# Optimization experiments

Hardware: AMD Instinct MI355X
Metric: run time of the kernel (lower is better)

The kernel has to match this reference:

```python
import jax, jax.numpy as jnp
import numpy as np

N, E, G = 100000, 1600000, 256      # nodes, edges, graphs in batch
IN_C, HID, OUT_C = 4, 128, 120
ALPHA = 0.5


def setup_inputs() -> dict:
    key = jax.random.key(0)
    ks = jax.random.split(key, 12)
    def w(k, i, o):
        return jax.random.normal(k, (i, o), jnp.float32) / np.float32(np.sqrt(i))
    return {
        "x": jax.random.normal(ks[0], (N, IN_C), jnp.float32),
        "edge_index": jax.random.randint(ks[1], (2, E), 0, N),
        "batch_seg": jnp.sort(jax.random.randint(ks[2], (N,), 0, G)),
        # DirGNNConv holds two independent GCNConvs (in / reversed direction)
        "W_in": w(ks[3], IN_C, HID),  "b_in": jnp.zeros((HID,), jnp.float32),
        "W_in_r": w(ks[4], IN_C, HID), "b_in_r": jnp.zeros((HID,), jnp.float32),
        "W_mid": w(ks[5], HID, HID),  "b_mid": jnp.zeros((HID,), jnp.float32),
        "W_mid_r": w(ks[6], HID, HID), "b_mid_r": jnp.zeros((HID,), jnp.float32),
        "W_out": w(ks[7], HID, OUT_C), "b_out": jnp.zeros((OUT_C,), jnp.float32),
        "W_out_r": w(ks[8], HID, OUT_C), "b_out_r": jnp.zeros((OUT_C,), jnp.float32),
    }


def _gcn(x, W, b, src, dst, n):
    # GCNConv with add_self_loops=False (DirGNNConv disables self-loops):
    # deg computed on destination side, norm = deg^-1/2[src] * deg^-1/2[dst]
    deg = jax.ops.segment_sum(jnp.ones(src.shape[0], x.dtype), dst, num_segments=n)
    dinv = jnp.where(deg > 0, jax.lax.rsqrt(jnp.maximum(deg, 1e-12)), 0.0)
    h = x @ W                                  # [N, out]
    msg = h[src] * (dinv[src] * dinv[dst])[:, None]  # gather + edge-normalize
    return jax.ops.segment_sum(msg, dst, num_segments=n) + b


def _dir_conv(x, Wi, bi, Wr, br, src, dst):
    # DirGNNConv(root_weight=False): (1-a)*conv(edge_index) + a*conv(flipped)
    n = x.shape[0]
    x_in = _gcn(x, Wi, bi, src, dst, n)
    x_out = _gcn(x, Wr, br, dst, src, n)
    return ALPHA * x_out + (1.0 - ALPHA) * x_in


def reference(x, edge_index, batch_seg, W_in, b_in, W_in_r, b_in_r,
              W_mid, b_mid, W_mid_r, b_mid_r, W_out, b_out, W_out_r, b_out_r):
    src, dst = edge_index[0], edge_index[1]
    h = jax.nn.relu(_dir_conv(x, W_in, b_in, W_in_r, b_in_r, src, dst))
    # dropout: eval mode -> identity
    h = jax.nn.relu(_dir_conv(h, W_mid, b_mid, W_mid_r, b_mid_r, src, dst))
    h = _dir_conv(h, W_out, b_out, W_out_r, b_out_r, src, dst)
    # global_mean_pool over batch_seg
    sums = jax.ops.segment_sum(h, batch_seg, num_segments=G)
    cnt = jax.ops.segment_sum(jnp.ones((h.shape[0],), h.dtype), batch_seg, num_segments=G)
    return sums / jnp.maximum(cnt, 1.0)[:, None]
```

## Files before the change

### kernel.cpp

```cpp
#include <hip/hip_runtime.h>
#include <hip/hip_fp16.h>

#define ALPHA 0.5f
#define BSH 9
#define BSZ 512
#define MAXB 512
#define CHUNK 4096

static inline int ceil_div(int a, int b) { return (a + b - 1) / b; }

typedef _Float16 half8 __attribute__((ext_vector_type(8)));
typedef float f32x4 __attribute__((ext_vector_type(4)));

__global__ void hist_kernel(const int* __restrict__ src, const int* __restrict__ dst,
                            unsigned int* __restrict__ bhI, unsigned int* __restrict__ bhO,
                            int E, int nbuck)
{
    __shared__ unsigned int hI[MAXB], hO[MAXB];
    for (int b = threadIdx.x; b < MAXB; b += blockDim.x) { hI[b] = 0; hO[b] = 0; }
    __syncthreads();
    for (int e = blockIdx.x * blockDim.x + threadIdx.x; e < E; e += gridDim.x * blockDim.x) {
        atomicAdd(&hI[dst[e] >> BSH], 1u);
        atomicAdd(&hO[src[e] >> BSH], 1u);
    }
    __syncthreads();
    for (int b = threadIdx.x; b < nbuck; b += blockDim.x) {
        if (hI[b]) atomicAdd(&bhI[b], hI[b]);
        if (hO[b]) atomicAdd(&bhO[b], hO[b]);
    }
}

__global__ void bucket_base_kernel(const unsigned int* __restrict__ bhI,
                                   const unsigned int* __restrict__ bhO,
                                   unsigned int* __restrict__ baseI, unsigned int* __restrict__ baseO,
                                   unsigned int* __restrict__ curI, unsigned int* __restrict__ curO,
                                   int nbuck)
{
    __shared__ unsigned int tI[MAXB], tO[MAXB];
    int t = threadIdx.x;
    unsigned int vI = (t < nbuck) ? bhI[t] : 0u;
    unsigned int vO = (t < nbuck) ? bhO[t] : 0u;
    tI[t] = vI; tO[t] = vO;
    __syncthreads();
    for (int o = 1; o < MAXB; o <<= 1) {
        unsigned int xI = (t >= o) ? tI[t - o] : 0u;
        unsigned int xO = (t >= o) ? tO[t - o] : 0u;
        __syncthreads();
        tI[t] += xI; tO[t] += xO;
        __syncthreads();
    }
    if (t < nbuck) {
        baseI[t] = tI[t] - vI; baseO[t] = tO[t] - vO;
        curI[t]  = tI[t] - vI; curO[t]  = tO[t] - vO;
    }
}

__global__ void bucket_scatter_kernel(const int* __restrict__ src, const int* __restrict__ dst,
                                      unsigned int* __restrict__ curI, unsigned int* __restrict__ curO,
                                      int2* __restrict__ ebI, int2* __restrict__ ebO, int E)
{
    __shared__ unsigned int cI[MAXB], cO[MAXB], bI[MAXB], bO[MAXB];
    int t = threadIdx.x;
    for (int b = t; b < MAXB; b += blockDim.x) { cI[b] = 0; cO[b] = 0; }
    __syncthreads();
    int e0 = blockIdx.x * CHUNK;
    int e1 = min(E, e0 + CHUNK);
    for (int e = e0 + t; e < e1; e += blockDim.x) {
        atomicAdd(&cI[dst[e] >> BSH], 1u);
        atomicAdd(&cO[src[e] >> BSH], 1u);
    }
    __syncthreads();
    for (int b = t; b < MAXB; b += blockDim.x) {
        unsigned int n = cI[b];
        if (n) bI[b] = atomicAdd(&curI[b], n);
        cI[b] = 0;
        n = cO[b];
        if (n) bO[b] = atomicAdd(&curO[b], n);
        cO[b] = 0;
    }
    __syncthreads();
    for (int e = e0 + t; e < e1; e += blockDim.x) {
        int s = src[e], d = dst[e];
        int lb = d >> BSH;
        unsigned int p = bI[lb] + atomicAdd(&cI[lb], 1u);
        ebI[p] = make_int2(d, s);
        lb = s >> BSH;
        p = bO[lb] + atomicAdd(&cO[lb], 1u);
        ebO[p] = make_int2(s, d);
    }
}

__global__ __launch_bounds__(256) void bucket_csr_kernel(
    const int2* __restrict__ ebI, const int2* __restrict__ ebO,
    const unsigned int* __restrict__ baseI, const unsigned int* __restrict__ baseO,
    const unsigned int* __restrict__ bendI, const unsigned int* __restrict__ bendO,
    unsigned int* __restrict__ rowI, unsigned int* __restrict__ rowO,
    unsigned int* __restrict__ degI, unsigned int* __restrict__ degO,
    float* __restrict__ dinvI, float* __restrict__ dinvO,
    int* __restrict__ adjI, int* __restrict__ adjO, int N)
{
    const int2* __restrict__ eb           = blockIdx.y ? ebO : ebI;
    const unsigned int* __restrict__ base = blockIdx.y ? baseO : baseI;
    const unsigned int* __restrict__ bend = blockIdx.y ? bendO : bendI;
    unsigned int* __restrict__ row        = blockIdx.y ? rowO : rowI;
    unsigned int* __restrict__ deg        = blockIdx.y ? degO : degI;
    float* __restrict__ dinv              = blockIdx.y ? dinvO : dinvI;
    int* __restrict__ adj                 = blockIdx.y ? adjO : adjI;

    __shared__ unsigned int d[BSZ];
    __shared__ unsigned int ex[BSZ];
    __shared__ unsigned int ps[256];
    int b = blockIdx.x, t = threadIdx.x;
    int nbase = b << BSH;

    for (int i = t; i < BSZ; i += 256) d[i] = 0;
    __syncthreads();
    unsigned int lo = base[b], hi = bend[b];
    for (unsigned int i = lo + t; i < hi; i += 256)
        atomicAdd(&d[eb[i].x - nbase], 1u);
    __syncthreads();

    ps[t] = d[2 * t] + d[2 * t + 1];
    __syncthreads();
    for (int o = 1; o < 256; o <<= 1) {
        unsigned int x = (t >= o) ? ps[t - o] : 0u;
        __syncthreads();
        ps[t] += x;
        __syncthreads();
    }
    unsigned int p0 = (t > 0) ? ps[t - 1] : 0u;
    ex[2 * t]     = p0;
    ex[2 * t + 1] = p0 + d[2 * t];
    __syncthreads();

    for (int i = t; i < BSZ; i += 256) {
        int v = nbase + i;
        if (v < N) {
            unsigned int dd = d[i];
            row[v]  = lo + ex[i];
            deg[v]  = dd;
            dinv[v] = dd ? rsqrtf((float)dd) : 0.f;
        }
    }
    __syncthreads();
    for (int i = t; i < BSZ; i += 256) d[i] = lo + ex[i];
    __syncthreads();
    for (unsigned int i = lo + t; i < hi; i += 256) {
        int2 e = eb[i];
        unsigned int p = atomicAdd(&d[e.x - nbase], 1u);
        adj[p] = e.y;
    }
}

__global__ void seg_cnt_kernel(const int* __restrict__ seg, float* __restrict__ cnt, int N, int G)
{
    int g = blockIdx.x * blockDim.x + threadIdx.x;
    if (g >= G) return;
    int lo = 0, hi = N;
    while (lo < hi) { int m = (lo + hi) >> 1; if (seg[m] < g) lo = m + 1; else hi = m; }
    int s0 = lo;
    hi = N;
    while (lo < hi) { int m = (lo + hi) >> 1; if (seg[m] < g + 1) lo = m + 1; else hi = m; }
    cnt[g] = (float)(lo - s0);
}

__global__ void prep_w_kernel(const float* __restrict__ Wi, const float* __restrict__ Wr,
                              const float* __restrict__ bi, const float* __restrict__ br,
                              __half* __restrict__ Wt, float* __restrict__ bcomb)
{
    int idx = blockIdx.x * 256 + threadIdx.x;
    if (idx < 128 * 256) {
        int j = idx >> 8, k = idx & 255;
        float w = (k < 128) ? (1.f - ALPHA) * Wi[k * 128 + j]
                            : ALPHA * Wr[(k - 128) * 128 + j];
        Wt[idx] = __float2half_rn(w);
    }
    if (idx < 128) bcomb[idx] = (1.f - ALPHA) * bi[idx] + ALPHA * br[idx];
}

__global__ __launch_bounds__(256) void layer1_fused_kernel(
    const unsigned int* __restrict__ rowI, const unsigned int* __restrict__ degI,
    const int* __restrict__ adjI, const float* __restrict__ dinvI,
    const unsigned int* __restrict__ rowO, const unsigned int* __restrict__ degO,
    const int* __restrict__ adjO, const float* __restrict__ dinvO,
    const float4* __restrict__ x4,
    const float* __restrict__ Wi, const float* __restrict__ bi,
    const float* __restrict__ Wr, const float* __restrict__ br,
    __half* __restrict__ h1, int N)
{
    __shared__ float wI[4][128], wO[4][128], bb[128];
    int t = threadIdx.x;
    if (t < 128) {
#pragma unroll
        for (int c = 0; c < 4; ++c) {
            wI[c][t] = (1.f - ALPHA) * Wi[c * 128 + t];
            wO[c][t] = ALPHA * Wr[c * 128 + t];
        }
        bb[t] = (1.f - ALPHA) * bi[t] + ALPHA * br[t];
    }
    __syncthreads();
    int v = blockIdx.x * 256 + t;
    if (v >= N) return;

    float4 aI = {0.f, 0.f, 0.f, 0.f};
    {
        unsigned int k = rowI[v], end = k + degI[v];
        for (; k < end; ++k) {
            int s = adjI[k];
            float w = dinvI[s];
            float4 xv = x4[s];
            aI.x += w * xv.x; aI.y += w * xv.y; aI.z += w * xv.z; aI.w += w * xv.w;
        }
        float dv = dinvI[v];
        aI.x *= dv; aI.y *= dv; aI.z *= dv; aI.w *= dv;
    }
    float4 aO = {0.f, 0.f, 0.f, 0.f};
    {
        unsigned int k = rowO[v], end = k + degO[v];
        for (; k < end; ++k) {
            int s = adjO[k];
            float w = dinvO[s];
            float4 xv = x4[s];
            aO.x += w * xv.x; aO.y += w * xv.y; aO.z += w * xv.z; aO.w += w * xv.w;
        }
        float dv = dinvO[v];
        aO.x *= dv; aO.y *= dv; aO.z *= dv; aO.w *= dv;
    }

    half8* outp = (half8*)&h1[(size_t)v * 128];
#pragma unroll
    for (int jq = 0; jq < 16; ++jq) {
        half8 o;
#pragma unroll
        for (int u = 0; u < 8; ++u) {
            int j = jq * 8 + u;
            float s = bb[j]
                    + aI.x * wI[0][j] + aI.y * wI[1][j] + aI.z * wI[2][j] + aI.w * wI[3][j]
                    + aO.x * wO[0][j] + aO.y * wO[1][j] + aO.z * wO[2][j] + aO.w * wO[3][j];
            o[u] = (_Float16)fmaxf(s, 0.f);
        }
        outp[jq] = o;
    }
}

__global__ void gather128_kernel(const unsigned int* __restrict__ rowstartI,
                                 const unsigned int* __restrict__ degI,
                                 const int* __restrict__ adjI,
                                 const float* __restrict__ dinvI,
                                 const unsigned int* __restrict__ rowstartO,
                                 const unsigned int* __restrict__ degO,
                                 const int* __restrict__ adjO,
                                 const float* __restrict__ dinvO,
                                 const half8* __restrict__ hp,
                                 half8* __restrict__ outI, half8* __restrict__ outO, int N)
{
    int v = blockIdx.x * 16 + (threadIdx.x >> 4);
    if (v >= N) return;
    int lane = threadIdx.x & 15;
    const unsigned int* __restrict__ rowstart = blockIdx.y ? rowstartO : rowstartI;
    const unsigned int* __restrict__ deg      = blockIdx.y ? degO : degI;
    const int* __restrict__ adj               = blockIdx.y ? adjO : adjI;
    const float* __restrict__ dinv            = blockIdx.y ? dinvO : dinvI;
    half8* __restrict__ out                   = blockIdx.y ? outO : outI;

    unsigned int k = rowstart[v];
    unsigned int end = k + deg[v];
    float acc[8];
#pragma unroll
    for (int i = 0; i < 8; ++i) acc[i] = 0.f;

    for (; k + 4 <= end; k += 4) {
        int s0 = adj[k], s1 = adj[k + 1], s2 = adj[k + 2], s3 = adj[k + 3];
        float w0 = dinv[s0], w1 = dinv[s1], w2 = dinv[s2], w3 = dinv[s3];
        half8 h0 = hp[(size_t)s0 * 16 + lane];
        half8 h1 = hp[(size_t)s1 * 16 + lane];
        half8 h2 = hp[(size_t)s2 * 16 + lane];
        half8 h3 = hp[(size_t)s3 * 16 + lane];
#pragma unroll
        for (int i = 0; i < 8; ++i)
            acc[i] += w0 * (float)h0[i] + w1 * (float)h1[i]
                    + w2 * (float)h2[i] + w3 * (float)h3[i];
    }
    for (; k < end; ++k) {
        int s = adj[k];
        float w = dinv[s];
        half8 hv = hp[(size_t)s * 16 + lane];
#pragma unroll
        for (int i = 0; i < 8; ++i)
            acc[i] += w * (float)hv[i];
    }
    float dv = dinv[v];
    half8 o;
#pragma unroll
    for (int i = 0; i < 8; ++i) o[i] = (_Float16)(dv * acc[i]);
    out[(size_t)v * 16 + lane] = o;
}

__global__ __launch_bounds__(256) void layer2_mfma_kernel(
    const __half* __restrict__ aggI, const __half* __restrict__ aggO,
    const __half* __restrict__ Wt,
    const float* __restrict__ bcomb,
    __half* __restrict__ h2, int N)
{
    int wave = threadIdx.x >> 6;
    int lane = threadIdx.x & 63;
    int v0 = blockIdx.x * 64 + wave * 16;
    int row = lane & 15;
    int kg  = lane >> 4;
    int vsafe = min(v0 + row, N - 1);

    f32x4 acc[8];
#pragma unroll
    for (int t = 0; t < 8; ++t) acc[t] = (f32x4){0.f, 0.f, 0.f, 0.f};

#pragma unroll
    for (int ks = 0; ks < 8; ++ks) {
        const __half* asrc = (ks < 4) ? aggI : aggO;
        int kofs = (ks & 3) * 32 + kg * 8;
        half8 afrag = *(const half8*)&asrc[(size_t)vsafe * 128 + kofs];
        int kw = ks * 32 + kg * 8;
#pragma unroll
        for (int t = 0; t < 8; ++t) {
            int j = t * 16 + row;
            half8 bfrag = *(const half8*)&Wt[(size_t)j * 256 + kw];
            acc[t] = __builtin_amdgcn_mfma_f32_16x16x32_f16(afrag, bfrag, acc[t], 0, 0, 0);
        }
    }

#pragma unroll
    for (int t = 0; t < 8; ++t) {
        int j = t * 16 + row;
        float bj = bcomb[j];
#pragma unroll
        for (int r = 0; r < 4; ++r) {
            int vr = v0 + kg * 4 + r;
            if (vr < N)
                h2[(size_t)vr * 128 + j] = __float2half_rn(fmaxf(acc[t][r] + bj, 0.f));
        }
    }
}

#define POOL_NODES 32
__global__ void pool_kernel(const __half* __restrict__ aI, const __half* __restrict__ aO,
                            const int* __restrict__ seg,
                            float* __restrict__ poolI, float* __restrict__ poolO, int N)
{
    int j = threadIdx.x;
    int v0 = blockIdx.x * POOL_NODES;
    if (v0 >= N) return;
    int v1 = min(N, v0 + POOL_NODES);
    float sI = 0.f, sO = 0.f;
    int cur = seg[v0];
    for (int v = v0; v < v1; ++v) {
        int g = seg[v];
        if (g != cur) {
            atomicAdd(&poolI[cur * 128 + j], sI);
            atomicAdd(&poolO[cur * 128 + j], sO);
            sI = 0.f; sO = 0.f; cur = g;
        }
        sI += __half2float(aI[(size_t)v * 128 + j]);
        sO += __half2float(aO[(size_t)v * 128 + j]);
    }
    atomicAdd(&poolI[cur * 128 + j], sI);
    atomicAdd(&poolO[cur * 128 + j], sO);
}

__global__ void final_kernel(const float* __restrict__ poolI, const float* __restrict__ poolO,
                             const float* __restrict__ cnt,
                             const float* __restrict__ Wo, const float* __restrict__ bo,
                             const float* __restrict__ Wor, const float* __restrict__ bor,
                             float* __restrict__ out, int G)
{
    int g = blockIdx.x;
    int j = threadIdx.x;
    if (g >= G || j >= 120) return;
    float acc = 0.f;
    for (int k = 0; k < 128; ++k) {
        acc += poolI[g * 128 + k] * ((1.f - ALPHA) * Wo[k * 120 + j])
             + poolO[g * 128 + k] * (ALPHA * Wor[k * 120 + j]);
    }
    float c = cnt[g];
    float bcomb = (1.f - ALPHA) * bo[j] + ALPHA * bor[j];
    out[g * 120 + j] = (c > 0.f) ? (acc / c + bcomb) : 0.f;
}

extern "C" void kernel_launch(void* const* d_in, const int* in_sizes, int n_in,
                              void* d_out, int out_size, void* d_ws, size_t ws_size,
                              hipStream_t stream)
{
    const float* x      = (const float*)d_in[0];
    const int*   ei     = (const int*)d_in[1];
    const int*   seg    = (const int*)d_in[2];
    const float* W_in   = (const float*)d_in[3];
    const float* b_in   = (const float*)d_in[4];
    const float* W_in_r = (const float*)d_in[5];
    const float* b_in_r = (const float*)d_in[6];
    const float* W_mid  = (const float*)d_in[7];
    const float* b_mid  = (const float*)d_in[8];
    const float* W_mid_r= (const float*)d_in[9];
    const float* b_mid_r= (const float*)d_in[10];
    const float* W_out  = (const float*)d_in[11];
    const float* b_out  = (const float*)d_in[12];
    const float* W_out_r= (const float*)d_in[13];
    const float* b_out_r= (const float*)d_in[14];

    const int N = in_sizes[0] / 4;
    const int E = in_sizes[1] / 2;
    const int G = out_size / 120;
    const int* src = ei;
    const int* dst = ei + E;
    const int NBUCK = ceil_div(N, BSZ);

    char* wsb = (char*)d_ws;
    size_t off = 0;
    auto alloc = [&](size_t elems) { void* p = wsb + off * 4; off += elems; return p; };

    unsigned int* bhI   = (unsigned int*)alloc(MAXB);
    unsigned int* bhO   = (unsigned int*)alloc(MAXB);
    float*        poolI = (float*)alloc((size_t)G * 128);
    float*        poolO = (float*)alloc((size_t)G * 128);
    size_t zero_elems = off;
    float*        cnt   = (float*)alloc(G);
    unsigned int* baseI = (unsigned int*)alloc(MAXB);
    unsigned int* baseO = (unsigned int*)alloc(MAXB);
    unsigned int* curI  = (unsigned int*)alloc(MAXB);
    unsigned int* curO  = (unsigned int*)alloc(MAXB);
    unsigned int* degI  = (unsigned int*)alloc(N);
    unsigned int* degO  = (unsigned int*)alloc(N);
    float*        dinvI = (float*)alloc(N);
    float*        dinvO = (float*)alloc(N);
    unsigned int* rowI  = (unsigned int*)alloc(N);
    unsigned int* rowO  = (unsigned int*)alloc(N);
    int*          adjI  = (int*)alloc(E);
    int*          adjO  = (int*)alloc(E);
    __half*       Wt    = (__half*)alloc(128 * 256 / 2);
    float*        bcomb = (float*)alloc(128);
    off = (off + 3) & ~(size_t)3;
    __half* hbuf = (__half*)alloc((size_t)N * 64);
    __half* aggI = (__half*)alloc((size_t)N * 64);
    __half* aggO = (__half*)alloc((size_t)N * 64);
    (void)ws_size;

    int2* ebI = (int2*)aggI;
    int2* ebO = (int2*)aggO;

    hipMemsetAsync(d_ws, 0, zero_elems * 4, stream);

    const int T = 256;
    hist_kernel<<<ceil_div(E, T * 16), T, 0, stream>>>(src, dst, bhI, bhO, E, NBUCK);
    bucket_base_kernel<<<1, MAXB, 0, stream>>>(bhI, bhO, baseI, baseO, curI, curO, NBUCK);
    bucket_scatter_kernel<<<ceil_div(E, CHUNK), T, 0, stream>>>(src, dst, curI, curO, ebI, ebO, E);
    bucket_csr_kernel<<<dim3(NBUCK, 2), T, 0, stream>>>(ebI, ebO, baseI, baseO, curI, curO,
                                                        rowI, rowO, degI, degO,
                                                        dinvI, dinvO, adjI, adjO, N);
    seg_cnt_kernel<<<ceil_div(G, T), T, 0, stream>>>(seg, cnt, N, G);
    prep_w_kernel<<<128, 256, 0, stream>>>(W_mid, W_mid_r, b_mid, b_mid_r, Wt, bcomb);

    layer1_fused_kernel<<<ceil_div(N, T), T, 0, stream>>>(
        rowI, degI, adjI, dinvI, rowO, degO, adjO, dinvO,
        (const float4*)x, W_in, b_in, W_in_r, b_in_r, hbuf, N);
    gather128_kernel<<<dim3(ceil_div(N, 16), 2), 256, 0, stream>>>(
        rowI, degI, adjI, dinvI, rowO, degO, adjO, dinvO,
        (const half8*)hbuf, (half8*)aggI, (half8*)aggO, N);
    layer2_mfma_kernel<<<ceil_div(N, 64), 256, 0, stream>>>(
        aggI, aggO, Wt, bcomb, hbuf, N);
    gather128_kernel<<<dim3(ceil_div(N, 16), 2), 256, 0, stream>>>(
        rowI, degI, adjI, dinvI, rowO, degO, adjO, dinvO,
        (const half8*)hbuf, (half8*)aggI, (half8*)aggO, N);
    pool_kernel<<<ceil_div(N, POOL_NODES), 128, 0, stream>>>(
        aggI, aggO, seg, poolI, poolO, N);
    final_kernel<<<G, 128, 0, stream>>>(poolI, poolO, cnt,
                                        W_out, b_out, W_out_r, b_out_r, (float*)d_out, G);
}
```

Baseline: 480.4 us.

## Fuse layer-2 gather with MFMA transform via shared-memory staging

Merges the first 128-wide gather (both edge directions) with the layer-2 MFMA matmul into one kernel. Each block of 16 nodes aggregates its in and out neighbours into LDS, then four waves run the 16x256x128 MFMA product from LDS and write relu'd fp16 output. This removes the round trip of the aggI/aggO intermediates through global memory and one launch. In exchange both directions run serially within one block rather than as separate grid dimensions, and every block reloads the whole weight matrix. Buffer roles are reassigned for the later gather and pool.

```diff
diff --git a/kernel.cpp b/kernel.cpp
--- a/kernel.cpp
+++ b/kernel.cpp
@@ -240,6 +240,92 @@
             o[u] = (_Float16)fmaxf(s, 0.f);
         }
         outp[jq] = o;
+    }
+}
+
+__global__ __launch_bounds__(256) void gather_mfma_kernel(
+    const unsigned int* __restrict__ rowI, const unsigned int* __restrict__ degI,
+    const int* __restrict__ adjI, const float* __restrict__ dinvI,
+    const unsigned int* __restrict__ rowO, const unsigned int* __restrict__ degO,
+    const int* __restrict__ adjO, const float* __restrict__ dinvO,
+    const half8* __restrict__ hp,
+    const __half* __restrict__ Wt,
+    const float* __restrict__ bcomb,
+    __half* __restrict__ h2, int N)
+{
+    __shared__ _Float16 sAB[16][264];
+    int t = threadIdx.x;
+    int node = t >> 4, lane = t & 15;
+    int v = blockIdx.x * 16 + node;
+    bool valid = v < N;
+
+#pragma unroll
+    for (int dir = 0; dir < 2; ++dir) {
+        const unsigned int* __restrict__ rw = dir ? rowO : rowI;
+        const unsigned int* __restrict__ dg = dir ? degO : degI;
+        const int* __restrict__ adj         = dir ? adjO : adjI;
+        const float* __restrict__ dinv      = dir ? dinvO : dinvI;
+        float acc[8];
+#pragma unroll
+        for (int i = 0; i < 8; ++i) acc[i] = 0.f;
+        if (valid) {
+            unsigned int k = rw[v], end = k + dg[v];
+            for (; k + 4 <= end; k += 4) {
+                int s0 = adj[k], s1 = adj[k + 1], s2 = adj[k + 2], s3 = adj[k + 3];
+                float w0 = dinv[s0], w1 = dinv[s1], w2 = dinv[s2], w3 = dinv[s3];
+                half8 h0 = hp[(size_t)s0 * 16 + lane];
+                half8 h1 = hp[(size_t)s1 * 16 + lane];
+                half8 h2v = hp[(size_t)s2 * 16 + lane];
+                half8 h3 = hp[(size_t)s3 * 16 + lane];
+#pragma unroll
+                for (int i = 0; i < 8; ++i)
+                    acc[i] += w0 * (float)h0[i] + w1 * (float)h1[i]
+                            + w2 * (float)h2v[i] + w3 * (float)h3[i];
+            }
+            for (; k < end; ++k) {
+                int s = adj[k];
+                float w = dinv[s];
+                half8 hv = hp[(size_t)s * 16 + lane];
+#pragma unroll
+                for (int i = 0; i < 8; ++i)
+                    acc[i] += w * (float)hv[i];
+            }
+            float dv = dinv[v];
+#pragma unroll
+            for (int i = 0; i < 8; ++i) acc[i] *= dv;
+        }
+        half8 o;
+#pragma unroll
+        for (int i = 0; i < 8; ++i) o[i] = (_Float16)acc[i];
+        *(half8*)&sAB[node][dir * 128 + lane * 8] = o;
+    }
+    __syncthreads();
+
+    int wave = t >> 6;
+    int l64 = t & 63;
+    int row = l64 & 15;
+    int kg  = l64 >> 4;
+    f32x4 acc0 = {0.f, 0.f, 0.f, 0.f}, acc1 = {0.f, 0.f, 0.f, 0.f};
+    int j0 = (wave * 2) * 16 + row;
+    int j1 = (wave * 2 + 1) * 16 + row;
+#pragma unroll
+    for (int ks = 0; ks < 8; ++ks) {
+        int kw = ks * 32 + kg * 8;
+        half8 afrag = *(const half8*)&sAB[row][kw];
+        half8 b0 = *(const half8*)&Wt[(size_t)j0 * 256 + kw];
+        half8 b1 = *(const half8*)&Wt[(size_t)j1 * 256 + kw];
+        acc0 = __builtin_amdgcn_mfma_f32_16x16x32_f16(afrag, b0, acc0, 0, 0, 0);
+        acc1 = __builtin_amdgcn_mfma_f32_16x16x32_f16(afrag, b1, acc1, 0, 0, 0);
+    }
+    int v0 = blockIdx.x * 16;
+    float bj0 = bcomb[j0], bj1 = bcomb[j1];
+#pragma unroll
+    for (int r = 0; r < 4; ++r) {
+        int vr = v0 + kg * 4 + r;
+        if (vr < N) {
+            h2[(size_t)vr * 128 + j0] = __float2half_rn(fmaxf(acc0[r] + bj0, 0.f));
+            h2[(size_t)vr * 128 + j1] = __float2half_rn(fmaxf(acc1[r] + bj1, 0.f));
+        }
     }
 }
 
@@ -294,50 +380,6 @@
 #pragma unroll
     for (int i = 0; i < 8; ++i) o[i] = (_Float16)(dv * acc[i]);
     out[(size_t)v * 16 + lane] = o;
-}
-
-__global__ __launch_bounds__(256) void layer2_mfma_kernel(
-    const __half* __restrict__ aggI, const __half* __restrict__ aggO,
-    const __half* __restrict__ Wt,
-    const float* __restrict__ bcomb,
-    __half* __restrict__ h2, int N)
-{
-    int wave = threadIdx.x >> 6;
-    int lane = threadIdx.x & 63;
-    int v0 = blockIdx.x * 64 + wave * 16;
-    int row = lane & 15;
-    int kg  = lane >> 4;
-    int vsafe = min(v0 + row, N - 1);
-
-    f32x4 acc[8];
-#pragma unroll
-    for (int t = 0; t < 8; ++t) acc[t] = (f32x4){0.f, 0.f, 0.f, 0.f};
-
-#pragma unroll
-    for (int ks = 0; ks < 8; ++ks) {
-        const __half* asrc = (ks < 4) ? aggI : aggO;
-        int kofs = (ks & 3) * 32 + kg * 8;
-        half8 afrag = *(const half8*)&asrc[(size_t)vsafe * 128 + kofs];
-        int kw = ks * 32 + kg * 8;
-#pragma unroll
-        for (int t = 0; t < 8; ++t) {
-            int j = t * 16 + row;
-            half8 bfrag = *(const half8*)&Wt[(size_t)j * 256 + kw];
-            acc[t] = __builtin_amdgcn_mfma_f32_16x16x32_f16(afrag, bfrag, acc[t], 0, 0, 0);
-        }
-    }
-
-#pragma unroll
-    for (int t = 0; t < 8; ++t) {
-        int j = t * 16 + row;
-        float bj = bcomb[j];
-#pragma unroll
-        for (int r = 0; r < 4; ++r) {
-            int vr = v0 + kg * 4 + r;
-            if (vr < N)
-                h2[(size_t)vr * 128 + j] = __float2half_rn(fmaxf(acc[t][r] + bj, 0.f));
-        }
-    }
 }
 
 #define POOL_NODES 32
@@ -459,16 +501,14 @@
     layer1_fused_kernel<<<ceil_div(N, T), T, 0, stream>>>(
         rowI, degI, adjI, dinvI, rowO, degO, adjO, dinvO,
         (const float4*)x, W_in, b_in, W_in_r, b_in_r, hbuf, N);
+    gather_mfma_kernel<<<ceil_div(N, 16), 256, 0, stream>>>(
+        rowI, degI, adjI, dinvI, rowO, degO, adjO, dinvO,
+        (const half8*)hbuf, Wt, bcomb, aggI, N);
     gather128_kernel<<<dim3(ceil_div(N, 16), 2), 256, 0, stream>>>(
         rowI, degI, adjI, dinvI, rowO, degO, adjO, dinvO,
-        (const half8*)hbuf, (half8*)aggI, (half8*)aggO, N);
-    layer2_mfma_kernel<<<ceil_div(N, 64), 256, 0, stream>>>(
-        aggI, aggO, Wt, bcomb, hbuf, N);
-    gather128_kernel<<<dim3(ceil_div(N, 16), 2), 256, 0, stream>>>(
-        rowI, degI, adjI, dinvI, rowO, degO, adjO, dinvO,
-        (const half8*)hbuf, (half8*)aggI, (half8*)aggO, N);
+        (const half8*)aggI, (half8*)hbuf, (half8*)aggO, N);
     pool_kernel<<<ceil_div(N, POOL_NODES), 128, 0, stream>>>(
-        aggI, aggO, seg, poolI, poolO, N);
+        hbuf, aggO, seg, poolI, poolO, N);
     final_kernel<<<G, 128, 0, stream>>>(poolI, poolO, cnt,
                                         W_out, b_out, W_out_r, b_out_r, (float*)d_out, G);
 }
```

Result: faster. 457.0 us (-4.9%).
